# Kernel optimization log

Hardware: AMD Instinct MI355X
Metric: run time of the kernel (lower is better)

The kernel has to match this reference:

```python
import jax, jax.numpy as jnp
import numpy as np

N, K, D = 32768, 8192, 64

def setup_inputs() -> dict:
    key = jax.random.key(0)
    kx, kc = jax.random.split(key)
    x = jax.random.normal(kx, (N, D), dtype=jnp.float32)
    codebook = jax.random.normal(kc, (K, D), dtype=jnp.float32)
    return {"x": x, "codebook": codebook}

def reference(x, codebook):
    # Faithful to: argmin(((codebook[None] - x[:, None])**2).sum(-1), -1)
    # Computed via the expanded squared distance to avoid the [N, K, D]
    # constant per row and does not affect argmin, but we include it so the
    # distance matrix matches the original math exactly.
    x_sq = jnp.sum(x * x, axis=-1, keepdims=True)          # [N, 1]
    c_sq = jnp.sum(codebook * codebook, axis=-1)           # [K]
    cross = jnp.einsum('nd,kd->nk', x, codebook)           # [N, K]
    dists = x_sq - 2.0 * cross + c_sq[None, :]             # [N, K]
    return jnp.argmin(dists, axis=-1)                      # [N] int32
```

## Files before the change

kernel.cpp:

```cpp
#include <hip/hip_runtime.h>
#include <math.h>


typedef __attribute__((ext_vector_type(8)))  _Float16 h8v;
typedef __attribute__((ext_vector_type(16))) float f16v;

constexpr int NROWS = 32768;
constexpr int KC    = 8192;
constexpr int DD    = 64;
constexpr int TPB   = 256;
constexpr int PTPB  = 256;
constexpr int BROWS = 64;
constexpr int BTILE = 128;
constexpr int NT    = KC / BTILE;
constexpr int TILE_HALFS = BTILE * DD * 2;
constexpr int BUF_HALFS  = TILE_HALFS + 256;

__device__ __forceinline__ void split2h(float v, _Float16& h1, _Float16& h2) {
  const float av = fabsf(v);
  _Float16 a = (_Float16)v;
  if (av < 6.1035156e-5f) a = (_Float16)0.f;
  h1 = a;
  h2 = (_Float16)((v - (float)a) * 4096.f);
}

__device__ __forceinline__ void gload_lds16(const void* g, void* l) {
  __builtin_amdgcn_global_load_lds(
      (const __attribute__((address_space(1))) void*)g,
      (__attribute__((address_space(3))) void*)l, 16, 0, 0);
}
__device__ __forceinline__ void gload_lds4(const void* g, void* l) {
  __builtin_amdgcn_global_load_lds(
      (const __attribute__((address_space(1))) void*)g,
      (__attribute__((address_space(3))) void*)l, 4, 0, 0);
}

__device__ __forceinline__ unsigned fkey(float f) {
  const unsigned u = __float_as_uint(f);
  return u ^ (((unsigned)((int)u >> 31)) | 0x80000000u);
}

__global__ void vq_pre_kernel(const float* __restrict__ cb,
                              _Float16* __restrict__ bSwz,
                              float* __restrict__ csq) {
  const int gidx = blockIdx.x * PTPB + threadIdx.x;
  const int code = gidx >> 2;
  const int kc4  = gidx & 3;
  const float* cp = cb + (size_t)code * DD + kc4 * 16;
  float v[16];
#pragma unroll
  for (int d = 0; d < 16; d += 4) {
    const float4 g = *(const float4*)(cp + d);
    v[d] = g.x; v[d + 1] = g.y; v[d + 2] = g.z; v[d + 3] = g.w;
  }
  float s = 0.f;
#pragma unroll
  for (int d = 0; d < 16; ++d) s = fmaf(v[d], v[d], s);
  s += __shfl_xor(s, 1, 64);
  s += __shfl_xor(s, 2, 64);
  if (kc4 == 0) csq[code] = s;
  _Float16 p1[16], p2[16];
#pragma unroll
  for (int d = 0; d < 16; ++d) split2h(v[d], p1[d], p2[d]);
  const int g = code >> 5, l = code & 31;
  _Float16* base = bSwz + (size_t)g * 4096;
#pragma unroll
  for (int p = 0; p < 2; ++p) {
    const _Float16* pl = p ? p2 : p1;
#pragma unroll
    for (int h = 0; h < 2; ++h) {
      h8v wv;
#pragma unroll
      for (int j = 0; j < 8; ++j) wv[j] = pl[h * 8 + j];
      *(h8v*)(base + (p * 4 + kc4) * 512 + (h * 32 + l) * 8) = wv;
    }
  }
}

__global__ __launch_bounds__(TPB, 2)
void vq_mfma_kernel(const float* __restrict__ x, const _Float16* __restrict__ bSwz,
                    const float* __restrict__ csq_g, int* __restrict__ out) {
  __shared__ alignas(16) _Float16 ldsBf[2 * BUF_HALFS];
  __shared__ alignas(16) unsigned long long ldsRed[BROWS][4];

  const int tid  = threadIdx.x;
  const int lane = tid & 63;
  const int w    = tid >> 6;
  const int half = lane >> 5;
  const int col  = lane & 31;
  const int wcode = w * 32 + col;
  const int blockRow = blockIdx.x * BROWS;

  {
    const _Float16* gs = bSwz + tid * 8;
    _Float16* ld = ldsBf + tid * 8;
#pragma unroll
    for (int seg = 0; seg < 8; ++seg)
      gload_lds16(gs + seg * 2048, ld + seg * 2048);
    if (w == 0) {
      float* cslot = (float*)(ldsBf + TILE_HALFS);
      gload_lds4(csq_g + lane, cslot);
      gload_lds4(csq_g + 64 + lane, cslot + 64);
    }
  }

  _Float16* ldsA = ldsBf + BUF_HALFS;
  {
    const int row = tid >> 2, dseg = (tid & 3) * 16;
    const float* xp = x + (size_t)(blockRow + row) * DD + dseg;
    float v[16];
#pragma unroll
    for (int d = 0; d < 16; d += 4) {
      const float4 g = *(const float4*)(xp + d);
      v[d] = g.x; v[d + 1] = g.y; v[d + 2] = g.z; v[d + 3] = g.w;
    }
    _Float16 qa[16], qb[16];
#pragma unroll
    for (int e = 0; e < 16; ++e) split2h(v[e], qa[e], qb[e]);
#pragma unroll
    for (int h2 = 0; h2 < 2; ++h2) {
      h8v a, b;
#pragma unroll
      for (int j = 0; j < 8; ++j) { a[j] = qa[h2 * 8 + j]; b[j] = qb[h2 * 8 + j]; }
      const int slot = (tid & 3) * 2 + h2;
      *(h8v*)&ldsA[(0 * 64 + row) * 64 + (slot ^ (row & 7)) * 8] = a;
      *(h8v*)&ldsA[(1 * 64 + row) * 64 + (slot ^ (row & 7)) * 8] = b;
    }
  }
  asm volatile("s_waitcnt lgkmcnt(0)\n\ts_barrier" ::: "memory");

  h8v afr[2][2][4];
#pragma unroll
  for (int q = 0; q < 2; ++q)
#pragma unroll
    for (int p = 0; p < 2; ++p)
#pragma unroll
      for (int kc = 0; kc < 4; ++kc) {
        const int arow = q * 32 + col;
        const int slot = kc * 2 + half;
        afr[q][p][kc] =
            *(const h8v*)&ldsA[(p * 64 + arow) * 64 + ((slot ^ (arow & 7))) * 8];
      }
  asm volatile("s_waitcnt vmcnt(0) lgkmcnt(0)\n\ts_barrier" ::: "memory");

  float bestD[32];
  unsigned bestC[32];
  float foldP[32];
#pragma unroll
  for (int i = 0; i < 32; ++i) {
    bestD[i] = INFINITY; bestC[i] = 0u; foldP[i] = -INFINITY;
  }
  float csP = 0.f;
  unsigned codeP = 0u;

  const f16v Z = {0.f,0.f,0.f,0.f,0.f,0.f,0.f,0.f,0.f,0.f,0.f,0.f,0.f,0.f,0.f,0.f};

#pragma unroll 2
  for (int t = 0; t < NT; ++t) {
    const int buf = t & 1;
    const _Float16* bp = ldsBf + buf * BUF_HALFS;
    if (t + 1 < NT) {
      const _Float16* gs = bSwz + (size_t)(t + 1) * TILE_HALFS + tid * 8;
      _Float16* ld = ldsBf + (buf ^ 1) * BUF_HALFS + tid * 8;
#pragma unroll
      for (int seg = 0; seg < 8; ++seg)
        gload_lds16(gs + seg * 2048, ld + seg * 2048);
      if (w == 0) {
        float* cslot = (float*)(ldsBf + (buf ^ 1) * BUF_HALFS + TILE_HALFS);
        gload_lds4(csq_g + (t + 1) * BTILE + lane, cslot);
        gload_lds4(csq_g + (t + 1) * BTILE + 64 + lane, cslot + 64);
      }
    }
    const _Float16* rb = bp + w * 4096 + lane * 8;
    h8v b0[4], b1[4];
#pragma unroll
    for (int kc = 0; kc < 4; ++kc) {
      b0[kc] = *(const h8v*)(rb + kc * 512);
      b1[kc] = *(const h8v*)(rb + (4 + kc) * 512);
    }
    const float cs = ((const float*)(bp + TILE_HALFS))[wcode];

    __builtin_amdgcn_s_setprio(1);
    f16v A0 = Z, B0v = Z, A1 = Z, B1v = Z;
#pragma unroll
    for (int kc = 0; kc < 4; ++kc) {
      A0  = __builtin_amdgcn_mfma_f32_32x32x16_f16(afr[0][0][kc], b0[kc], A0,  0, 0, 0);
      A1  = __builtin_amdgcn_mfma_f32_32x32x16_f16(afr[1][0][kc], b0[kc], A1,  0, 0, 0);
      B0v = __builtin_amdgcn_mfma_f32_32x32x16_f16(afr[0][0][kc], b1[kc], B0v, 0, 0, 0);
      B1v = __builtin_amdgcn_mfma_f32_32x32x16_f16(afr[1][0][kc], b1[kc], B1v, 0, 0, 0);
    }
#pragma unroll
    for (int kc = 0; kc < 4; ++kc) {
      B0v = __builtin_amdgcn_mfma_f32_32x32x16_f16(afr[0][1][kc], b0[kc], B0v, 0, 0, 0);
      B1v = __builtin_amdgcn_mfma_f32_32x32x16_f16(afr[1][1][kc], b0[kc], B1v, 0, 0, 0);
    }
    __builtin_amdgcn_s_setprio(0);

#pragma unroll
    for (int i = 0; i < 32; ++i) {
      const float d_ = fmaf(-2.f, foldP[i], csP);
      if (d_ < bestD[i]) { bestD[i] = d_; bestC[i] = codeP; }
    }
#pragma unroll
    for (int i = 0; i < 16; ++i) {
      foldP[i]      = fmaf(B0v[i], 2.44140625e-4f, A0[i]);
      foldP[16 + i] = fmaf(B1v[i], 2.44140625e-4f, A1[i]);
    }
    csP = cs;
    codeP = (unsigned)(t * BTILE) + wcode;

    asm volatile("s_waitcnt vmcnt(0) lgkmcnt(0)\n\ts_barrier" ::: "memory");
  }
#pragma unroll
  for (int i = 0; i < 32; ++i) {
    const float d_ = fmaf(-2.f, foldP[i], csP);
    if (d_ < bestD[i]) { bestD[i] = d_; bestC[i] = codeP; }
  }

  unsigned long long key[32];
#pragma unroll
  for (int i = 0; i < 32; ++i)
    key[i] = ((unsigned long long)fkey(bestD[i]) << 32) | bestC[i];
#pragma unroll
  for (int i = 0; i < 32; ++i) {
#pragma unroll
    for (int m = 1; m < 32; m <<= 1) {
      const unsigned long long o = __shfl_xor(key[i], m, 64);
      if (o < key[i]) key[i] = o;
    }
  }
  if (col == 0) {
#pragma unroll
    for (int i = 0; i < 32; ++i) {
      const int ii = i & 15, q = i >> 4;
      const int row = q * 32 + (ii & 3) + 8 * (ii >> 2) + 4 * half;
      ldsRed[row][w] = key[i];
    }
  }
  __syncthreads();
  if (tid < BROWS) {
    unsigned long long a = ldsRed[tid][0];
    const unsigned long long b = ldsRed[tid][1];
    const unsigned long long c = ldsRed[tid][2];
    const unsigned long long d = ldsRed[tid][3];
    if (b < a) a = b;
    if (c < a) a = c;
    if (d < a) a = d;
    out[blockRow + tid] = (int)(unsigned)(a & 0xFFFFFFFFull);
  }
}

extern "C" void kernel_launch(void* const* d_in, const int* in_sizes, int n_in,
                              void* d_out, int out_size, void* d_ws, size_t ws_size,
                              hipStream_t stream) {
  const float* x  = (const float*)d_in[0];
  const float* cb = (const float*)d_in[1];
  int* out = (int*)d_out;

  _Float16* bSwz = (_Float16*)d_ws;
  float* csq_g = (float*)((char*)d_ws + (size_t)KC * DD * 2 * 2);

  vq_pre_kernel<<<dim3(KC * 4 / PTPB), dim3(PTPB), 0, stream>>>(cb, bSwz, csq_g);
  vq_mfma_kernel<<<dim3(NROWS / BROWS), dim3(TPB), 0, stream>>>(
      x, bSwz, csq_g, out);
}
```

Baseline: 177.6 us.

## Give each wave private double-buffered codebook slices and drop block barriers

The codebook layout now packs each 32-code group together with its squared norms, duplicated into 64 floats, so one wave can fetch its whole unit with a single load sequence. Each wave streams and double-buffers its own slice of LDS and waits only on its own vmcnt, which removes the block-wide s_barrier from every tile iteration. The distance fold is now computed right after the MFMAs, and the compare is delayed by one iteration. The trade-offs are a larger LDS footprint from the per-wave buffers and less latency hiding, since each wave now blocks on its own load before each step.

```diff
diff --git a/kernel.cpp b/kernel.cpp
--- a/kernel.cpp
+++ b/kernel.cpp
@@ -11,10 +11,8 @@
 constexpr int TPB   = 256;
 constexpr int PTPB  = 256;
 constexpr int BROWS = 64;
-constexpr int BTILE = 128;
-constexpr int NT    = KC / BTILE;
-constexpr int TILE_HALFS = BTILE * DD * 2;
-constexpr int BUF_HALFS  = TILE_HALFS + 256;
+constexpr int GUNIT = 4224;
+constexpr int NBODY = 64;
 
 __device__ __forceinline__ void split2h(float v, _Float16& h1, _Float16& h2) {
   const float av = fabsf(v);
@@ -41,8 +39,7 @@
 }
 
 __global__ void vq_pre_kernel(const float* __restrict__ cb,
-                              _Float16* __restrict__ bSwz,
-                              float* __restrict__ csq) {
+                              _Float16* __restrict__ bSwz) {
   const int gidx = blockIdx.x * PTPB + threadIdx.x;
   const int code = gidx >> 2;
   const int kc4  = gidx & 3;
@@ -58,12 +55,11 @@
   for (int d = 0; d < 16; ++d) s = fmaf(v[d], v[d], s);
   s += __shfl_xor(s, 1, 64);
   s += __shfl_xor(s, 2, 64);
-  if (kc4 == 0) csq[code] = s;
   _Float16 p1[16], p2[16];
 #pragma unroll
   for (int d = 0; d < 16; ++d) split2h(v[d], p1[d], p2[d]);
   const int g = code >> 5, l = code & 31;
-  _Float16* base = bSwz + (size_t)g * 4096;
+  _Float16* base = bSwz + (size_t)g * GUNIT;
 #pragma unroll
   for (int p = 0; p < 2; ++p) {
     const _Float16* pl = p ? p2 : p1;
@@ -75,12 +71,16 @@
       *(h8v*)(base + (p * 4 + kc4) * 512 + (h * 32 + l) * 8) = wv;
     }
   }
+  if (kc4 == 0) {
+    float* cs2 = (float*)(base + 4096);
+    cs2[l] = s; cs2[32 + l] = s;
+  }
 }
 
 __global__ __launch_bounds__(TPB, 2)
 void vq_mfma_kernel(const float* __restrict__ x, const _Float16* __restrict__ bSwz,
-                    const float* __restrict__ csq_g, int* __restrict__ out) {
-  __shared__ alignas(16) _Float16 ldsBf[2 * BUF_HALFS];
+                    int* __restrict__ out) {
+  __shared__ alignas(16) _Float16 ldsBf[2 * 4 * GUNIT];
   __shared__ alignas(16) unsigned long long ldsRed[BROWS][4];
 
   const int tid  = threadIdx.x;
@@ -88,23 +88,9 @@
   const int w    = tid >> 6;
   const int half = lane >> 5;
   const int col  = lane & 31;
-  const int wcode = w * 32 + col;
   const int blockRow = blockIdx.x * BROWS;
 
-  {
-    const _Float16* gs = bSwz + tid * 8;
-    _Float16* ld = ldsBf + tid * 8;
-#pragma unroll
-    for (int seg = 0; seg < 8; ++seg)
-      gload_lds16(gs + seg * 2048, ld + seg * 2048);
-    if (w == 0) {
-      float* cslot = (float*)(ldsBf + TILE_HALFS);
-      gload_lds4(csq_g + lane, cslot);
-      gload_lds4(csq_g + 64 + lane, cslot + 64);
-    }
-  }
-
-  _Float16* ldsA = ldsBf + BUF_HALFS;
+  _Float16* ldsA = ldsBf;
   {
     const int row = tid >> 2, dseg = (tid & 3) * 16;
     const float* xp = x + (size_t)(blockRow + row) * DD + dseg;
@@ -141,44 +127,50 @@
         afr[q][p][kc] =
             *(const h8v*)&ldsA[(p * 64 + arow) * 64 + ((slot ^ (arow & 7))) * 8];
       }
-  asm volatile("s_waitcnt vmcnt(0) lgkmcnt(0)\n\ts_barrier" ::: "memory");
+  asm volatile("s_waitcnt lgkmcnt(0)\n\ts_barrier" ::: "memory");
+
+  {
+    const _Float16* gs = bSwz + (size_t)w * GUNIT;
+    _Float16* ld = ldsBf + w * GUNIT;
+#pragma unroll
+    for (int c = 0; c < 8; ++c)
+      gload_lds16(gs + c * 512 + lane * 8, ld + c * 512 + lane * 8);
+    gload_lds4((const float*)(gs + 4096) + lane, (float*)(ld + 4096));
+  }
 
   float bestD[32];
   unsigned bestC[32];
-  float foldP[32];
+  float distP[32];
 #pragma unroll
   for (int i = 0; i < 32; ++i) {
-    bestD[i] = INFINITY; bestC[i] = 0u; foldP[i] = -INFINITY;
-  }
-  float csP = 0.f;
+    bestD[i] = INFINITY; bestC[i] = 0u; distP[i] = INFINITY;
+  }
   unsigned codeP = 0u;
 
   const f16v Z = {0.f,0.f,0.f,0.f,0.f,0.f,0.f,0.f,0.f,0.f,0.f,0.f,0.f,0.f,0.f,0.f};
 
-#pragma unroll 2
-  for (int t = 0; t < NT; ++t) {
-    const int buf = t & 1;
-    const _Float16* bp = ldsBf + buf * BUF_HALFS;
-    if (t + 1 < NT) {
-      const _Float16* gs = bSwz + (size_t)(t + 1) * TILE_HALFS + tid * 8;
-      _Float16* ld = ldsBf + (buf ^ 1) * BUF_HALFS + tid * 8;
-#pragma unroll
-      for (int seg = 0; seg < 8; ++seg)
-        gload_lds16(gs + seg * 2048, ld + seg * 2048);
-      if (w == 0) {
-        float* cslot = (float*)(ldsBf + (buf ^ 1) * BUF_HALFS + TILE_HALFS);
-        gload_lds4(csq_g + (t + 1) * BTILE + lane, cslot);
-        gload_lds4(csq_g + (t + 1) * BTILE + 64 + lane, cslot + 64);
-      }
-    }
-    const _Float16* rb = bp + w * 4096 + lane * 8;
+  for (int t = 0; t < NBODY; ++t) {
+    asm volatile("s_waitcnt vmcnt(0)" ::: "memory");
+    if (t + 1 < NBODY) {
+      const _Float16* gs = bSwz + (size_t)((t + 1) * 4 + w) * GUNIT;
+      _Float16* ld = ldsBf + ((t + 1) & 1) * (4 * GUNIT) + w * GUNIT;
+#pragma unroll
+      for (int c = 0; c < 8; ++c)
+        gload_lds16(gs + c * 512 + lane * 8, ld + c * 512 + lane * 8);
+      gload_lds4((const float*)(gs + 4096) + lane, (float*)(ld + 4096));
+    }
+    const _Float16* rb = ldsBf + (t & 1) * (4 * GUNIT) + w * GUNIT;
     h8v b0[4], b1[4];
 #pragma unroll
     for (int kc = 0; kc < 4; ++kc) {
-      b0[kc] = *(const h8v*)(rb + kc * 512);
-      b1[kc] = *(const h8v*)(rb + (4 + kc) * 512);
-    }
-    const float cs = ((const float*)(bp + TILE_HALFS))[wcode];
+      b0[kc] = *(const h8v*)(rb + kc * 512 + lane * 8);
+      b1[kc] = *(const h8v*)(rb + (4 + kc) * 512 + lane * 8);
+    }
+    const float cs = ((const float*)(rb + 4096))[lane];
+
+#pragma unroll
+    for (int i = 0; i < 32; ++i)
+      if (distP[i] < bestD[i]) { bestD[i] = distP[i]; bestC[i] = codeP; }
 
     __builtin_amdgcn_s_setprio(1);
     f16v A0 = Z, B0v = Z, A1 = Z, B1v = Z;
@@ -197,25 +189,15 @@
     __builtin_amdgcn_s_setprio(0);
 
 #pragma unroll
-    for (int i = 0; i < 32; ++i) {
-      const float d_ = fmaf(-2.f, foldP[i], csP);
-      if (d_ < bestD[i]) { bestD[i] = d_; bestC[i] = codeP; }
-    }
-#pragma unroll
     for (int i = 0; i < 16; ++i) {
-      foldP[i]      = fmaf(B0v[i], 2.44140625e-4f, A0[i]);
-      foldP[16 + i] = fmaf(B1v[i], 2.44140625e-4f, A1[i]);
-    }
-    csP = cs;
-    codeP = (unsigned)(t * BTILE) + wcode;
-
-    asm volatile("s_waitcnt vmcnt(0) lgkmcnt(0)\n\ts_barrier" ::: "memory");
-  }
-#pragma unroll
-  for (int i = 0; i < 32; ++i) {
-    const float d_ = fmaf(-2.f, foldP[i], csP);
-    if (d_ < bestD[i]) { bestD[i] = d_; bestC[i] = codeP; }
-  }
+      distP[i]      = fmaf(-2.f, fmaf(B0v[i], 2.44140625e-4f, A0[i]), cs);
+      distP[16 + i] = fmaf(-2.f, fmaf(B1v[i], 2.44140625e-4f, A1[i]), cs);
+    }
+    codeP = (unsigned)((t * 4 + w) * 32 + col);
+  }
+#pragma unroll
+  for (int i = 0; i < 32; ++i)
+    if (distP[i] < bestD[i]) { bestD[i] = distP[i]; bestC[i] = codeP; }
 
   unsigned long long key[32];
 #pragma unroll
@@ -258,9 +240,7 @@
   int* out = (int*)d_out;
 
   _Float16* bSwz = (_Float16*)d_ws;
-  float* csq_g = (float*)((char*)d_ws + (size_t)KC * DD * 2 * 2);
-
-  vq_pre_kernel<<<dim3(KC * 4 / PTPB), dim3(PTPB), 0, stream>>>(cb, bSwz, csq_g);
-  vq_mfma_kernel<<<dim3(NROWS / BROWS), dim3(TPB), 0, stream>>>(
-      x, bSwz, csq_g, out);
-}
+
+  vq_pre_kernel<<<dim3(KC * 4 / PTPB), dim3(PTPB), 0, stream>>>(cb, bSwz);
+  vq_mfma_kernel<<<dim3(NROWS / BROWS), dim3(TPB), 0, stream>>>(x, bSwz, out);
+}
```

Result: no change. 179.0 us (+0.8%).
